# Optimization experiments

Hardware: AMD Instinct MI355X
Metric: run time of the kernel (lower is better)

Reference implementation:

```python
import jax, jax.numpy as jnp
import numpy as np

N = 50000        # nodes
E = 800000       # edges (avg degree 16)
IN_DIM = 256
H = 8            # heads
D = 32           # out_dim per head
T = 4            # edge_type_num
F = 16           # edge_feature_dim
NEG_SLOPE = 0.2


def setup_inputs() -> dict:
    key = jax.random.key(0)
    ks = jax.random.split(key, 9)
    feat = jax.random.normal(ks[0], (N, IN_DIM), dtype=jnp.float32)
    e_pro = jax.random.normal(ks[1], (E, F), dtype=jnp.float32)
    mask = jax.random.uniform(ks[2], (E, T), dtype=jnp.float32)
    W_n = jax.random.normal(ks[3], (IN_DIM, H * D), dtype=jnp.float32) * (1.0 / np.sqrt(IN_DIM))
    attn_l = jax.random.normal(ks[4], (H, D, T), dtype=jnp.float32) * 0.1
    attn_r = jax.random.normal(ks[5], (H, D, T), dtype=jnp.float32) * 0.1
    attn_m = jax.random.normal(ks[6], (H, F, T), dtype=jnp.float32) * 0.1
    src = jax.random.randint(ks[7], (E,), 0, N, dtype=jnp.int32)
    dst = jax.random.randint(ks[8], (E,), 0, N, dtype=jnp.int32)
    return {"feat": feat, "e_pro": e_pro, "mask": mask, "W_n": W_n,
            "attn_l": attn_l, "attn_r": attn_r, "attn_m": attn_m,
            "src": src, "dst": dst}


def reference(feat, e_pro, mask, W_n, attn_l, attn_r, attn_m, src, dst):
    # node projection: [N, H, D]
    feat_src = (feat @ W_n).reshape(N, H, D)

    # per-node attention logits per edge type: [N, H, T]
    el = jnp.einsum("nhd,hdt->nht", feat_src, attn_l)
    er = jnp.einsum("nhd,hdt->nht", feat_src, attn_r)
    # per-edge logits per edge type: [E, H, T]
    em = jnp.einsum("ef,hft->eht", e_pro, attn_m)

    # bmm with edge-type mask [E, T] -> scalar per head: [E, H]
    left = jnp.einsum("eht,et->eh", el[src], mask)
    right = jnp.einsum("eht,et->eh", er[dst], mask)
    em_e = jnp.einsum("eht,et->eh", em, mask)

    e = (left + right + em_e) / 3.0
    e = jnp.where(e > 0, e, NEG_SLOPE * e)  # leaky_relu

    # edge softmax over incoming edges of each dst node (stable)
    e_max = jax.ops.segment_max(e, dst, num_segments=N)          # [N, H]
    e_exp = jnp.exp(e - e_max[dst])                               # [E, H]
    e_sum = jax.ops.segment_sum(e_exp, dst, num_segments=N)      # [N, H]
    a = e_exp / e_sum[dst]                                       # [E, H]

    # u_mul_e + sum aggregation: [E, H, D] -> [N, H, D]
    msg = feat_src[src] * a[:, :, None]
    rst = jax.ops.segment_sum(msg, dst, num_segments=N)

    # cat=True: concat heads
    return rst.reshape(N, H * D)
```

## Files before the change

### kernel.cpp

```cpp
#include <hip/hip_runtime.h>
#include <hip/hip_bf16.h>
#include <hip/hip_fp16.h>

#define NN 50000
#define NEDGE 800000
#define INDIM 256
#define NH 8
#define ND 32
#define HD 256
#define NT 4
#define NF 16

typedef __attribute__((ext_vector_type(8))) short s16x8;
typedef __attribute__((ext_vector_type(4))) float f32x4;
typedef unsigned short u16;

__device__ __forceinline__ float bf2f(u16 u) {
    return __uint_as_float(((unsigned int)u) << 16);
}
__device__ __forceinline__ u16 f2bf(float f) {
    __hip_bfloat16 h = __float2bfloat16(f);
    return *reinterpret_cast<u16*>(&h);
}
__device__ __forceinline__ u16 f2h(float f) {
    __half h = __float2half(f);
    return *reinterpret_cast<u16*>(&h);
}
__device__ __forceinline__ float h2f(u16 u) {
    __half h = *reinterpret_cast<__half*>(&u);
    return __half2float(h);
}

__global__ __launch_bounds__(256) void prep_kernel(const float* __restrict__ W,
                                                   u16* __restrict__ Wt,
                                                   int* __restrict__ cnt,
                                                   int* __restrict__ cursor)
{
    int idx = blockIdx.x * 256 + threadIdx.x;
    int k = idx >> 8, c = idx & 255;
    Wt[(size_t)c * 256 + k] = f2bf(W[idx]);
    if (idx < NN) { cnt[idx] = 0; cursor[idx] = 0; }
}

__global__ void hist_kernel(const int* __restrict__ dst, int* __restrict__ cnt, int ne) {
    int e = blockIdx.x * 256 + threadIdx.x;
    if (e < ne) atomicAdd(&cnt[dst[e]], 1);
}

__global__ __launch_bounds__(256) void gemm_mfma(
    const float* __restrict__ feat, const u16* __restrict__ Wt,
    u16* __restrict__ fs, int nrows)
{
    const int tid = threadIdx.x;
    __shared__ u16 At[32 * 256];
    const int brow = blockIdx.x * 32;

    #pragma unroll
    for (int it = 0; it < 4; ++it) {
        int fo = it * 2048 + tid * 8;
        int row = fo >> 8, col = fo & 255;
        int grow = brow + row;
        if (grow >= nrows) grow = nrows - 1;
        const float* gp = feat + (size_t)grow * 256 + col;
        float4 x = *reinterpret_cast<const float4*>(gp);
        float4 y = *reinterpret_cast<const float4*>(gp + 4);
        s16x8 v;
        v[0] = (short)f2bf(x.x); v[1] = (short)f2bf(x.y);
        v[2] = (short)f2bf(x.z); v[3] = (short)f2bf(x.w);
        v[4] = (short)f2bf(y.x); v[5] = (short)f2bf(y.y);
        v[6] = (short)f2bf(y.z); v[7] = (short)f2bf(y.w);
        int byte = (col * 2) ^ ((row & 7) << 4);
        *reinterpret_cast<s16x8*>((char*)At + row * 512 + byte) = v;
    }
    __syncthreads();

    const int wave = tid >> 6, lane = tid & 63;
    const int c0 = wave * 64;
    const int rA = lane & 15;
    const int kg = lane >> 4;

    f32x4 acc[2][4] = {};

    for (int k0 = 0; k0 < 256; k0 += 32) {
        const int kk = k0 + kg * 8;
        const int byte = (kk * 2) ^ ((rA & 7) << 4);
        s16x8 a0 = *reinterpret_cast<const s16x8*>((char*)At + rA * 512 + byte);
        s16x8 a1 = *reinterpret_cast<const s16x8*>((char*)At + (16 + rA) * 512 + byte);
        #pragma unroll
        for (int ct = 0; ct < 4; ++ct) {
            s16x8 b = *reinterpret_cast<const s16x8*>(Wt + (size_t)(c0 + ct * 16 + rA) * 256 + kk);
            acc[0][ct] = __builtin_amdgcn_mfma_f32_16x16x32_bf16(a0, b, acc[0][ct], 0, 0, 0);
            acc[1][ct] = __builtin_amdgcn_mfma_f32_16x16x32_bf16(a1, b, acc[1][ct], 0, 0, 0);
        }
    }

    #pragma unroll
    for (int rt = 0; rt < 2; ++rt) {
        #pragma unroll
        for (int r = 0; r < 4; ++r) {
            int row = brow + rt * 16 + kg * 4 + r;
            if (row < nrows) {
                #pragma unroll
                for (int ct = 0; ct < 4; ++ct) {
                    fs[(size_t)row * 256 + c0 + ct * 16 + rA] = f2bf(acc[rt][ct][r]);
                }
            }
        }
    }
}

__global__ __launch_bounds__(256) void elr_kernel(
    const u16* __restrict__ fs,
    const float* __restrict__ attn_l, const float* __restrict__ attn_r,
    u16* __restrict__ el, u16* __restrict__ er, int n)
{
    __shared__ float s_al[NH * ND * NT];
    __shared__ float s_ar[NH * ND * NT];
    for (int i = threadIdx.x; i < NH * ND * NT; i += 256) {
        s_al[i] = attn_l[i];
        s_ar[i] = attn_r[i];
    }
    __syncthreads();
    int wv = threadIdx.x >> 6, lane = threadIdx.x & 63;
    int node = blockIdx.x * 4 + wv;
    if (node >= n) return;
    int h = lane >> 3, j0 = (lane & 7) * 4;
    ushort4 u = *reinterpret_cast<const ushort4*>(fs + (size_t)node * HD + lane * 4);
    float f0 = bf2f(u.x), f1 = bf2f(u.y), f2 = bf2f(u.z), f3 = bf2f(u.w);
    const float* al = s_al + h * (ND * NT) + j0 * NT;
    const float* ar = s_ar + h * (ND * NT) + j0 * NT;
    float pl[NT], pr[NT];
    #pragma unroll
    for (int t = 0; t < NT; ++t) {
        pl[t] = f0*al[t] + f1*al[NT + t] + f2*al[2*NT + t] + f3*al[3*NT + t];
        pr[t] = f0*ar[t] + f1*ar[NT + t] + f2*ar[2*NT + t] + f3*ar[3*NT + t];
    }
    #pragma unroll
    for (int d = 1; d < 8; d <<= 1) {
        #pragma unroll
        for (int t = 0; t < NT; ++t) {
            pl[t] += __shfl_xor(pl[t], d);
            pr[t] += __shfl_xor(pr[t], d);
        }
    }
    if ((lane & 7) == 0) {
        ushort4 ol, orr;
        ol.x = f2h(pl[0]); ol.y = f2h(pl[1]); ol.z = f2h(pl[2]); ol.w = f2h(pl[3]);
        orr.x = f2h(pr[0]); orr.y = f2h(pr[1]); orr.z = f2h(pr[2]); orr.w = f2h(pr[3]);
        *reinterpret_cast<ushort4*>(el + (size_t)node * (NH*NT) + h * NT) = ol;
        *reinterpret_cast<ushort4*>(er + (size_t)node * (NH*NT) + h * NT) = orr;
    }
}

__global__ void scan1_kernel(const int* __restrict__ cnt, int* __restrict__ off,
                             int* __restrict__ blksum, int n) {
    __shared__ int sm[256];
    int i = blockIdx.x * 256 + threadIdx.x;
    int v = (i < n) ? cnt[i] : 0;
    sm[threadIdx.x] = v;
    __syncthreads();
    for (int d = 1; d < 256; d <<= 1) {
        int t = (threadIdx.x >= d) ? sm[threadIdx.x - d] : 0;
        __syncthreads();
        sm[threadIdx.x] += t;
        __syncthreads();
    }
    if (i < n) off[i] = sm[threadIdx.x] - v;
    if (threadIdx.x == 255) blksum[blockIdx.x] = sm[255];
}

__global__ void scan2_kernel(int* blksum, int nb) {
    __shared__ int sm[256];
    int v = (threadIdx.x < nb) ? blksum[threadIdx.x] : 0;
    sm[threadIdx.x] = v;
    __syncthreads();
    for (int d = 1; d < 256; d <<= 1) {
        int t = (threadIdx.x >= d) ? sm[threadIdx.x - d] : 0;
        __syncthreads();
        sm[threadIdx.x] += t;
        __syncthreads();
    }
    blksum[threadIdx.x] = sm[threadIdx.x] - v;
}

__global__ void scan3_kernel(int* __restrict__ off, const int* __restrict__ blksum,
                             int n, int ne) {
    int i = blockIdx.x * 256 + threadIdx.x;
    if (i < n) off[i] += blksum[blockIdx.x];
    if (i == 0) off[n] = ne;
}

__global__ __launch_bounds__(256) void fill_edge_kernel(
    const float* __restrict__ e_pro, const float* __restrict__ mask,
    const float* __restrict__ attn_m,
    const int* __restrict__ src, const int* __restrict__ dst,
    const u16* __restrict__ el, const u16* __restrict__ er,
    const int* __restrict__ off, int* __restrict__ cursor,
    int2* __restrict__ es, u16* __restrict__ ev, int ne)
{
    const int bid = blockIdx.x;
    const int tid = threadIdx.x;

    if (bid % 9 == 0) {
        int e = (bid / 9) * 256 + tid;
        if (e < ne) {
            int d = dst[e];
            int p = atomicAdd(&cursor[d], 1);
            es[off[d] + p] = make_int2(e, src[e]);
        }
        return;
    }

    const int ebid = bid - 1 - bid / 9;
    __shared__ float4 s_am4[NF][NH];
    const int eb = ebid * 32;
    const int j = tid & 7;
    const int e = eb + (tid >> 3);

    int s = src[e], d = dst[e];
    union { uint2 v; u16 u[4]; } lv, rv;
    lv.v = *reinterpret_cast<const uint2*>(el + (size_t)s * (NH*NT) + j * NT);
    rv.v = *reinterpret_cast<const uint2*>(er + (size_t)d * (NH*NT) + j * NT);
    float4 mk = *reinterpret_cast<const float4*>(mask + (size_t)e * NT);
    float2 myep = *reinterpret_cast<const float2*>(e_pro + (size_t)e * NF + j * 2);

    for (int i = tid; i < NH * NF; i += 256) {
        int h = i >> 4, f = i & 15;
        s_am4[f][h] = *reinterpret_cast<const float4*>(attn_m + (size_t)h * (NF * NT) + f * NT);
    }
    __syncthreads();

    const int gbase = (tid & 63) & 56;
    float pa = myep.x, pb = myep.y;
    float em = 0.f;
    #pragma unroll
    for (int f = 0; f < NF; ++f) {
        float4 am = s_am4[f][j];
        float amm = mk.x*am.x + mk.y*am.y + mk.z*am.z + mk.w*am.w;
        float epv = __shfl((f & 1) ? pb : pa, gbase | (f >> 1));
        em = fmaf(epv, amm, em);
    }
    float left  = mk.x*h2f(lv.u[0]) + mk.y*h2f(lv.u[1]) + mk.z*h2f(lv.u[2]) + mk.w*h2f(lv.u[3]);
    float right = mk.x*h2f(rv.u[0]) + mk.y*h2f(rv.u[1]) + mk.z*h2f(rv.u[2]) + mk.w*h2f(rv.u[3]);

    float v = (left + right + em) * (1.0f / 3.0f);
    v = v > 0.f ? v : 0.2f * v;
    ev[(size_t)e * NH + j] = f2h(__expf(v));
}

__global__ __launch_bounds__(256) void agg_kernel(
    const int* __restrict__ off, const int2* __restrict__ es,
    const u16* __restrict__ ev, const u16* __restrict__ fs,
    float* __restrict__ out, int n)
{
    int wv = threadIdx.x >> 6, lane = threadIdx.x & 63;
    int node = blockIdx.x * 4 + wv;
    if (node >= n) return;
    int beg = off[node], end = off[node + 1];
    int deg = end - beg;

    int h = lane & 7, sub = lane >> 3;
    float vc[8];
    int sc[8];
    #pragma unroll
    for (int slot = 0; slot < 8; ++slot) {
        int i = beg + slot * 8 + sub;
        float v = 0.f; int sn = 0;
        if (i < end) {
            int2 p = es[i];
            v = h2f(ev[(size_t)p.x * NH + h]);
            sn = p.y;
        }
        vc[slot] = v; sc[slot] = sn;
    }

    int h2 = lane >> 3;
    const int col = lane * 4;
    float a0 = 0.f, a1 = 0.f, a2 = 0.f, a3 = 0.f, sw = 0.f;
    int deg_ = deg < 64 ? deg : 64;
    int nchunk = (deg_ + 7) >> 3;
    #pragma unroll
    for (int c = 0; c < 8; ++c) {
        if (c >= nchunk) break;
        float w8 = vc[c];
        int s8 = sc[c];
        float w[8]; int sn[8];
        #pragma unroll
        for (int q = 0; q < 8; ++q) {
            w[q]  = __shfl(w8, q * 8 + h2);
            sn[q] = __shfl(s8, q * 8 + h2);
        }
        ushort4 u[8];
        #pragma unroll
        for (int q = 0; q < 8; ++q)
            u[q] = *reinterpret_cast<const ushort4*>(fs + (size_t)sn[q] * HD + col);
        #pragma unroll
        for (int q = 0; q < 8; ++q) {
            sw += w[q];
            a0 = fmaf(w[q], bf2f(u[q].x), a0);
            a1 = fmaf(w[q], bf2f(u[q].y), a1);
            a2 = fmaf(w[q], bf2f(u[q].z), a2);
            a3 = fmaf(w[q], bf2f(u[q].w), a3);
        }
    }
    for (int i = beg + 64; i < end; ++i) {
        int2 p = es[i];
        float w = h2f(ev[(size_t)p.x * NH + h2]);
        sw += w;
        ushort4 u = *reinterpret_cast<const ushort4*>(fs + (size_t)p.y * HD + col);
        a0 = fmaf(w, bf2f(u.x), a0); a1 = fmaf(w, bf2f(u.y), a1);
        a2 = fmaf(w, bf2f(u.z), a2); a3 = fmaf(w, bf2f(u.w), a3);
    }
    float invS = sw > 0.f ? 1.f / sw : 0.f;
    a0 *= invS; a1 *= invS; a2 *= invS; a3 *= invS;
    *reinterpret_cast<float4*>(&out[(size_t)node * HD + col]) = make_float4(a0, a1, a2, a3);
}

extern "C" void kernel_launch(void* const* d_in, const int* in_sizes, int n_in,
                              void* d_out, int out_size, void* d_ws, size_t ws_size,
                              hipStream_t stream)
{
    const float* feat   = (const float*)d_in[0];
    const float* e_pro  = (const float*)d_in[1];
    const float* mask   = (const float*)d_in[2];
    const float* W_n    = (const float*)d_in[3];
    const float* attn_l = (const float*)d_in[4];
    const float* attn_r = (const float*)d_in[5];
    const float* attn_m = (const float*)d_in[6];
    const int* src      = (const int*)d_in[7];
    const int* dst      = (const int*)d_in[8];
    float* out = (float*)d_out;

    char* ws = (char*)d_ws;
    size_t o = 0;
    auto alloc = [&](size_t bytes) -> void* {
        void* p = (void*)(ws + o);
        o += (bytes + 255) & ~(size_t)255;
        return p;
    };
    u16* fs     = (u16*)alloc((size_t)NN * HD * 2);
    u16* Wt     = (u16*)alloc((size_t)INDIM * HD * 2);
    u16* el     = (u16*)alloc((size_t)NN * NH * NT * 2);
    u16* er     = (u16*)alloc((size_t)NN * NH * NT * 2);
    u16* ev     = (u16*)alloc((size_t)NEDGE * NH * 2);
    int2* es    = (int2*)alloc((size_t)NEDGE * 8);
    int* cnt    = (int*)alloc((size_t)NN * 4);
    int* cursor = (int*)alloc((size_t)NN * 4);
    int* offs   = (int*)alloc((size_t)(NN + 1) * 4);
    int* blksum = (int*)alloc(256 * 4);
    (void)ws_size; (void)in_sizes; (void)n_in; (void)out_size;

    dim3 b256(256);
    hipLaunchKernelGGL(prep_kernel, dim3(256), b256, 0, stream, W_n, Wt, cnt, cursor);
    hipLaunchKernelGGL(hist_kernel, dim3((NEDGE + 255) / 256), b256, 0, stream, dst, cnt, NEDGE);
    hipLaunchKernelGGL(gemm_mfma, dim3((NN + 31) / 32), b256, 0, stream, feat, Wt, fs, NN);
    hipLaunchKernelGGL(scan1_kernel, dim3((NN + 255) / 256), b256, 0, stream, cnt, offs, blksum, NN);
    hipLaunchKernelGGL(scan2_kernel, dim3(1), b256, 0, stream, blksum, (NN + 255) / 256);
    hipLaunchKernelGGL(scan3_kernel, dim3((NN + 255) / 256), b256, 0, stream, offs, blksum, NN, NEDGE);
    hipLaunchKernelGGL(elr_kernel, dim3((NN + 3) / 4), b256, 0, stream, fs, attn_l, attn_r, el, er, NN);
    hipLaunchKernelGGL(fill_edge_kernel, dim3(9 * 3125), b256, 0, stream,
                       e_pro, mask, attn_m, src, dst, el, er, offs, cursor, es, ev, NEDGE);
    hipLaunchKernelGGL(agg_kernel, dim3((NN + 3) / 4), b256, 0, stream,
                       offs, es, ev, fs, out, NN);
}
```

Before: 242.0 us.

## Fuse degree histogram into GEMM and software-pipeline gather loads in aggregation

```diff
diff --git a/kernel.cpp b/kernel.cpp
--- a/kernel.cpp
+++ b/kernel.cpp
@@ -42,16 +42,18 @@
     if (idx < NN) { cnt[idx] = 0; cursor[idx] = 0; }
 }
 
-__global__ void hist_kernel(const int* __restrict__ dst, int* __restrict__ cnt, int ne) {
-    int e = blockIdx.x * 256 + threadIdx.x;
-    if (e < ne) atomicAdd(&cnt[dst[e]], 1);
-}
-
 __global__ __launch_bounds__(256) void gemm_mfma(
     const float* __restrict__ feat, const u16* __restrict__ Wt,
+    const int* __restrict__ dst, int* __restrict__ cnt,
     u16* __restrict__ fs, int nrows)
 {
     const int tid = threadIdx.x;
+    {
+        int e0 = (blockIdx.x * 256 + tid) * 2;
+        if (e0 < NEDGE)     atomicAdd(&cnt[dst[e0]], 1);
+        if (e0 + 1 < NEDGE) atomicAdd(&cnt[dst[e0 + 1]], 1);
+    }
+
     __shared__ u16 At[32 * 256];
     const int brow = blockIdx.x * 32;
 
@@ -224,8 +226,8 @@
     float4 mk = *reinterpret_cast<const float4*>(mask + (size_t)e * NT);
     float2 myep = *reinterpret_cast<const float2*>(e_pro + (size_t)e * NF + j * 2);
 
-    for (int i = tid; i < NH * NF; i += 256) {
-        int h = i >> 4, f = i & 15;
+    if (tid < 128) {
+        int f = tid >> 3, h = tid & 7;
         s_am4[f][h] = *reinterpret_cast<const float4*>(attn_m + (size_t)h * (NF * NT) + f * NT);
     }
     __syncthreads();
@@ -279,28 +281,46 @@
     float a0 = 0.f, a1 = 0.f, a2 = 0.f, a3 = 0.f, sw = 0.f;
     int deg_ = deg < 64 ? deg : 64;
     int nchunk = (deg_ + 7) >> 3;
+
+    float wq[8]; int snq[8]; ushort4 uq[8];
+    if (nchunk > 0) {
+        #pragma unroll
+        for (int q = 0; q < 8; ++q) {
+            wq[q]  = __shfl(vc[0], q * 8 + h2);
+            snq[q] = __shfl(sc[0], q * 8 + h2);
+        }
+        #pragma unroll
+        for (int q = 0; q < 8; ++q)
+            uq[q] = *reinterpret_cast<const ushort4*>(fs + (size_t)snq[q] * HD + col);
+    }
     #pragma unroll
     for (int c = 0; c < 8; ++c) {
         if (c >= nchunk) break;
-        float w8 = vc[c];
-        int s8 = sc[c];
-        float w[8]; int sn[8];
+        float wn[8]; int snn[8]; ushort4 un[8];
+        bool more = (c + 1 < nchunk);
+        if (more) {
+            #pragma unroll
+            for (int q = 0; q < 8; ++q) {
+                wn[q]  = __shfl(vc[c + 1], q * 8 + h2);
+                snn[q] = __shfl(sc[c + 1], q * 8 + h2);
+            }
+            #pragma unroll
+            for (int q = 0; q < 8; ++q)
+                un[q] = *reinterpret_cast<const ushort4*>(fs + (size_t)snn[q] * HD + col);
+        }
         #pragma unroll
         for (int q = 0; q < 8; ++q) {
-            w[q]  = __shfl(w8, q * 8 + h2);
-            sn[q] = __shfl(s8, q * 8 + h2);
-        }
-        ushort4 u[8];
-        #pragma unroll
-        for (int q = 0; q < 8; ++q)
-            u[q] = *reinterpret_cast<const ushort4*>(fs + (size_t)sn[q] * HD + col);
-        #pragma unroll
-        for (int q = 0; q < 8; ++q) {
-            sw += w[q];
-            a0 = fmaf(w[q], bf2f(u[q].x), a0);
-            a1 = fmaf(w[q], bf2f(u[q].y), a1);
-            a2 = fmaf(w[q], bf2f(u[q].z), a2);
-            a3 = fmaf(w[q], bf2f(u[q].w), a3);
+            sw += wq[q];
+            a0 = fmaf(wq[q], bf2f(uq[q].x), a0);
+            a1 = fmaf(wq[q], bf2f(uq[q].y), a1);
+            a2 = fmaf(wq[q], bf2f(uq[q].z), a2);
+            a3 = fmaf(wq[q], bf2f(uq[q].w), a3);
+        }
+        if (more) {
+            #pragma unroll
+            for (int q = 0; q < 8; ++q) {
+                wq[q] = wn[q]; snq[q] = snn[q]; uq[q] = un[q];
+            }
         }
     }
     for (int i = beg + 64; i < end; ++i) {
@@ -352,12 +372,11 @@
 
     dim3 b256(256);
     hipLaunchKernelGGL(prep_kernel, dim3(256), b256, 0, stream, W_n, Wt, cnt, cursor);
-    hipLaunchKernelGGL(hist_kernel, dim3((NEDGE + 255) / 256), b256, 0, stream, dst, cnt, NEDGE);
-    hipLaunchKernelGGL(gemm_mfma, dim3((NN + 31) / 32), b256, 0, stream, feat, Wt, fs, NN);
+    hipLaunchKernelGGL(gemm_mfma, dim3((NN + 31) / 32), b256, 0, stream, feat, Wt, dst, cnt, fs, NN);
+    hipLaunchKernelGGL(elr_kernel, dim3((NN + 3) / 4), b256, 0, stream, fs, attn_l, attn_r, el, er, NN);
     hipLaunchKernelGGL(scan1_kernel, dim3((NN + 255) / 256), b256, 0, stream, cnt, offs, blksum, NN);
     hipLaunchKernelGGL(scan2_kernel, dim3(1), b256, 0, stream, blksum, (NN + 255) / 256);
     hipLaunchKernelGGL(scan3_kernel, dim3((NN + 255) / 256), b256, 0, stream, offs, blksum, NN, NEDGE);
-    hipLaunchKernelGGL(elr_kernel, dim3((NN + 3) / 4), b256, 0, stream, fs, attn_l, attn_r, el, er, NN);
     hipLaunchKernelGGL(fill_edge_kernel, dim3(9 * 3125), b256, 0, stream,
                        e_pro, mask, attn_m, src, dst, el, er, offs, cursor, es, ev, NEDGE);
     hipLaunchKernelGGL(agg_kernel, dim3((NN + 3) / 4), b256, 0, stream,
```

New measurement: 232.2 us. -4.1%, faster.
